# Kernel optimization log

Measured on AMD Instinct MI355X. Metric: run time of the kernel, lower is better.

The kernel has to match this reference:

```python
import jax, jax.numpy as jnp
import numpy as np

N_NODES = 50000
N_EDGES = 800000  # includes N_NODES self-loops so every node has in-degree >= 1
D_IN = 64
D_OUT = 64


def setup_inputs() -> dict:
    key = jax.random.key(0)
    k_feat, k_src, k_dst, k_wt, k_wp = jax.random.split(key, 5)
    feat = jax.random.normal(k_feat, (N_NODES, D_IN), dtype=jnp.float32)
    n_rand = N_EDGES - N_NODES
    loops = jnp.arange(N_NODES, dtype=jnp.int64)
    src = jnp.concatenate([loops, jax.random.randint(k_src, (n_rand,), 0, N_NODES, dtype=jnp.int64)])
    dst = jnp.concatenate([loops, jax.random.randint(k_dst, (n_rand,), 0, N_NODES, dtype=jnp.int64)])
    scale = 1.0 / np.sqrt(D_IN)
    W_theta = jax.random.normal(k_wt, (D_IN, D_OUT), dtype=jnp.float32) * scale
    b_theta = jnp.zeros((D_OUT,), dtype=jnp.float32)
    W_phi = jax.random.normal(k_wp, (D_IN, D_OUT), dtype=jnp.float32) * scale
    b_phi = jnp.zeros((D_OUT,), dtype=jnp.float32)
    return {"feat": feat, "src": src, "dst": dst,
            "W_theta": W_theta, "b_theta": b_theta,
            "W_phi": W_phi, "b_phi": b_phi}


def reference(feat, src, dst, W_theta, b_theta, W_phi, b_phi):
    # Per-edge message: theta(x_dst - x_src)  [fn.v_sub_u then Dense theta]
    diff = feat[dst] - feat[src]                       # [E, D_in]
    theta_e = diff @ W_theta + b_theta                 # [E, D_out]
    # Per-destination-node term: phi(x_dst)  [Dense phi]
    phi = feat @ W_phi + b_phi                         # [N, D_out]
    e = theta_e + phi[dst]                             # [E, D_out]  (fn.e_add_v)
    # Scatter-max aggregation by destination node (fn.max)
    out = jax.ops.segment_max(e, dst, num_segments=feat.shape[0])  # [N, D_out]
    return out
```

## Files before the change

### kernel.cpp

```cpp
#include <hip/hip_runtime.h>
#include <hip/hip_bf16.h>

#define N_NODES 50000
#define N_EDGES 800000
#define D 64
#define NB 391
#define BCAP 4096
#define CHUNK_E 2048
#define NSC 391
#define NSTRIP 3125
#define GEMM_BLKS 782

typedef __attribute__((ext_vector_type(8))) short short8v;
typedef __attribute__((ext_vector_type(4))) float float4v;

__device__ __forceinline__ float b2f(unsigned short h) {
    return __uint_as_float(((unsigned)h) << 16);
}
__device__ __forceinline__ unsigned short f2b(float f) {
    __hip_bfloat16 t = __float2bfloat16(f);
    return *reinterpret_cast<unsigned short*>(&t);
}
__device__ __forceinline__ short f2bs(float f) { return (short)f2b(f); }
__device__ __forceinline__ unsigned f2ord(float f) {
    unsigned u = __float_as_uint(f);
    return (u & 0x80000000u) ? ~u : (u | 0x80000000u);
}
__device__ __forceinline__ float ord2f(unsigned o) {
    return __uint_as_float((o & 0x80000000u) ? (o ^ 0x80000000u) : ~o);
}

__global__ __launch_bounds__(256)
void setup(const void* __restrict__ featv, const void* __restrict__ srcv,
           const void* __restrict__ Wtv, const void* __restrict__ btv,
           const void* __restrict__ Wpv, const void* __restrict__ bpv,
           unsigned* __restrict__ flags,
           unsigned short* __restrict__ WTfrag, unsigned short* __restrict__ WPfrag,
           float* __restrict__ bias_sum) {
    __shared__ unsigned sf[2];
    const int t = threadIdx.x;
    if (t < 64) {
        const unsigned short* p = (const unsigned short*)featv;
        float x = b2f(p[2 * t]);
        float a = fabsf(x);
        bool insane = !(a <= 64.f) || (x != 0.f && a < 9.3132e-10f);
        unsigned long long m = __ballot(insane);
        if (t == 0) sf[0] = (__popcll(m) >= 8) ? 1u : 0u;
    } else if (t < 128) {
        const int* s32 = (const int*)srcv;
        int v = s32[2 * (t - 64) + 1];
        unsigned long long m = __ballot(v == 0);
        if (t == 64) sf[1] = (__popcll(m) >= 32) ? 1u : 0u;
    }
    __syncthreads();
    const unsigned fp32mode = sf[0];
    if (t < 2) flags[t] = sf[t];
#pragma unroll
    for (int i = 0; i < 16; ++i) {
        int e = i * 256 + t;
        int k = e >> 6, n = e & 63;
        float vt, vp;
        if (fp32mode) {
            vt = ((const float*)Wtv)[e];
            vp = ((const float*)Wpv)[e];
        } else {
            vt = b2f(((const unsigned short*)Wtv)[e]);
            vp = b2f(((const unsigned short*)Wpv)[e]);
        }
        WTfrag[n * 64 + k] = f2b(vt);
        WPfrag[n * 64 + k] = f2b(vp);
    }
    if (t < 64) {
        if (fp32mode)
            bias_sum[t] = ((const float*)btv)[t] + ((const float*)bpv)[t];
        else
            bias_sum[t] = b2f(((const unsigned short*)btv)[t])
                        + b2f(((const unsigned short*)bpv)[t]);
    }
}

__global__ __launch_bounds__(256)
void gemm_scatter(const void* __restrict__ featv,
                  const unsigned short* __restrict__ WTfrag,
                  const unsigned short* __restrict__ WPfrag,
                  const float* __restrict__ bias_sum,
                  const void* __restrict__ srcv, const void* __restrict__ dstv,
                  const unsigned* __restrict__ flags,
                  unsigned* __restrict__ c_cur, unsigned* __restrict__ packed,
                  unsigned short* __restrict__ T16, void* __restrict__ outv) {
    const unsigned fp32mode = flags[0];
    if (blockIdx.x < GEMM_BLKS) {
        const int lane = threadIdx.x & 63;
        const int wid  = threadIdx.x >> 6;
        const int w = blockIdx.x * 4 + wid;
        if (w >= NSTRIP) return;
        const int m = lane & 15, q = lane >> 4;

        short8v A0, A1;
        if (fp32mode) {
            const float* fr = (const float*)featv + (w * 16 + m) * D + q * 8;
            float4 l0 = *(const float4*)(fr);
            float4 h0 = *(const float4*)(fr + 4);
            float4 l1 = *(const float4*)(fr + 32);
            float4 h1 = *(const float4*)(fr + 36);
            A0 = (short8v){f2bs(l0.x), f2bs(l0.y), f2bs(l0.z), f2bs(l0.w),
                           f2bs(h0.x), f2bs(h0.y), f2bs(h0.z), f2bs(h0.w)};
            A1 = (short8v){f2bs(l1.x), f2bs(l1.y), f2bs(l1.z), f2bs(l1.w),
                           f2bs(h1.x), f2bs(h1.y), f2bs(h1.z), f2bs(h1.w)};
        } else {
            const short* fr = (const short*)featv + (w * 16 + m) * D + q * 8;
            A0 = *(const short8v*)fr;
            A1 = *(const short8v*)(fr + 32);
        }

        const short8v* BT = (const short8v*)WTfrag;
        const short8v* BP = (const short8v*)WPfrag;
        float* Cf  = (float*)outv;
        unsigned short* Ch = (unsigned short*)outv;

#pragma unroll
        for (int c = 0; c < 4; ++c) {
            const int col = 16 * c + m;
            short8v Bt0 = BT[col * 8 + q];
            short8v Bt1 = BT[col * 8 + 4 + q];
            short8v Bp0 = BP[col * 8 + q];
            short8v Bp1 = BP[col * 8 + 4 + q];
            float bs = bias_sum[col];
            float4v accT = (float4v){0.f, 0.f, 0.f, 0.f};
            float4v accP = (float4v){bs, bs, bs, bs};
            accT = __builtin_amdgcn_mfma_f32_16x16x32_bf16(A0, Bt0, accT, 0, 0, 0);
            accT = __builtin_amdgcn_mfma_f32_16x16x32_bf16(A1, Bt1, accT, 0, 0, 0);
            accP = __builtin_amdgcn_mfma_f32_16x16x32_bf16(A0, Bp0, accP, 0, 0, 0);
            accP = __builtin_amdgcn_mfma_f32_16x16x32_bf16(A1, Bp1, accP, 0, 0, 0);
#pragma unroll
            for (int r = 0; r < 4; ++r) {
                const int row = w * 16 + q * 4 + r;
                T16[row * D + col] = f2b(accT[r]);
                if (fp32mode) Cf[row * D + col] = accT[r] + accP[r];
                else          Ch[row * D + col] = f2b(accT[r] + accP[r]);
            }
        }
    } else {
        __shared__ unsigned h[NB];
        const int t = threadIdx.x;
        for (int i = t; i < NB; i += 256) h[i] = 0;
        __syncthreads();
        const unsigned idx64 = flags[1];
        const int base = (blockIdx.x - GEMM_BLKS) * CHUNK_E;
        unsigned pk[CHUNK_E / 256];
#pragma unroll
        for (int j = 0; j < CHUNK_E / 256; ++j) {
            int e = base + j * 256 + t;
            unsigned p = 0xFFFFFFFFu;
            if (e < N_EDGES) {
                int s, d;
                if (idx64) {
                    s = (int)((const long long*)srcv)[e];
                    d = (int)((const long long*)dstv)[e];
                } else {
                    s = ((const int*)srcv)[e];
                    d = ((const int*)dstv)[e];
                }
                s = min(max(s, 0), N_NODES - 1);
                d = min(max(d, 0), N_NODES - 1);
                if (s != d) {
                    p = ((unsigned)d << 16) | (unsigned)s;
                    atomicAdd(&h[d >> 7], 1u);
                }
            }
            pk[j] = p;
        }
        __syncthreads();
        for (int i = t; i < NB; i += 256) h[i] = atomicAdd(&c_cur[i], h[i]);
        __syncthreads();
#pragma unroll
        for (int j = 0; j < CHUNK_E / 256; ++j) {
            unsigned p = pk[j];
            if (p != 0xFFFFFFFFu) {
                unsigned bkt = p >> 23;
                unsigned pos = atomicAdd(&h[bkt], 1u);
                if (pos < BCAP)
                    packed[bkt * BCAP + pos] = p;
            }
        }
    }
}

__global__ __launch_bounds__(512)
void bucket_min(const unsigned* __restrict__ c_cur, const unsigned* __restrict__ packed,
                const unsigned short* __restrict__ T16, const unsigned* __restrict__ flags,
                void* __restrict__ outv) {
    __shared__ unsigned mn[128 * 64];
    const unsigned fp32mode = flags[0];
    const int t = threadIdx.x;
    const int b = blockIdx.x;
    const int node0 = b << 7;
    for (int sl = t; sl < 128 * 16; sl += 512) {
        const int row = sl >> 4;
        const int f4 = (sl & 15) << 2;
        unsigned* mp = &mn[row * 64 + f4];
        if (node0 + row < N_NODES) {
            uint2 v = *(const uint2*)(T16 + (node0 + row) * D + f4);
            mp[0] = f2ord(b2f((unsigned short)v.x));
            mp[1] = f2ord(b2f((unsigned short)(v.x >> 16)));
            mp[2] = f2ord(b2f((unsigned short)v.y));
            mp[3] = f2ord(b2f((unsigned short)(v.y >> 16)));
        } else {
            mp[0] = mp[1] = mp[2] = mp[3] = 0xFFFFFFFFu;
        }
    }
    __syncthreads();
    const int cnt = min((int)c_cur[b], BCAP);
    const unsigned* pb = packed + b * BCAP;
    const int lane = t & 63, wv = t >> 6;
    const int g = lane >> 4, fb = (lane & 15) << 2;
    int i = wv * 4 + g;
    for (; i + 96 < cnt; i += 128) {
        unsigned p0 = pb[i],      p1 = pb[i + 32];
        unsigned p2 = pb[i + 64], p3 = pb[i + 96];
        uint2 v0 = *(const uint2*)(T16 + (int)(p0 & 0xFFFFu) * D + fb);
        uint2 v1 = *(const uint2*)(T16 + (int)(p1 & 0xFFFFu) * D + fb);
        uint2 v2 = *(const uint2*)(T16 + (int)(p2 & 0xFFFFu) * D + fb);
        uint2 v3 = *(const uint2*)(T16 + (int)(p3 & 0xFFFFu) * D + fb);
        unsigned* m0p = &mn[(int)((p0 >> 16) & 127u) * 64 + fb];
        unsigned* m1p = &mn[(int)((p1 >> 16) & 127u) * 64 + fb];
        unsigned* m2p = &mn[(int)((p2 >> 16) & 127u) * 64 + fb];
        unsigned* m3p = &mn[(int)((p3 >> 16) & 127u) * 64 + fb];
        atomicMin(m0p + 0, f2ord(b2f((unsigned short)v0.x)));
        atomicMin(m0p + 1, f2ord(b2f((unsigned short)(v0.x >> 16))));
        atomicMin(m0p + 2, f2ord(b2f((unsigned short)v0.y)));
        atomicMin(m0p + 3, f2ord(b2f((unsigned short)(v0.y >> 16))));
        atomicMin(m1p + 0, f2ord(b2f((unsigned short)v1.x)));
        atomicMin(m1p + 1, f2ord(b2f((unsigned short)(v1.x >> 16))));
        atomicMin(m1p + 2, f2ord(b2f((unsigned short)v1.y)));
        atomicMin(m1p + 3, f2ord(b2f((unsigned short)(v1.y >> 16))));
        atomicMin(m2p + 0, f2ord(b2f((unsigned short)v2.x)));
        atomicMin(m2p + 1, f2ord(b2f((unsigned short)(v2.x >> 16))));
        atomicMin(m2p + 2, f2ord(b2f((unsigned short)v2.y)));
        atomicMin(m2p + 3, f2ord(b2f((unsigned short)(v2.y >> 16))));
        atomicMin(m3p + 0, f2ord(b2f((unsigned short)v3.x)));
        atomicMin(m3p + 1, f2ord(b2f((unsigned short)(v3.x >> 16))));
        atomicMin(m3p + 2, f2ord(b2f((unsigned short)v3.y)));
        atomicMin(m3p + 3, f2ord(b2f((unsigned short)(v3.y >> 16))));
    }
    for (; i < cnt; i += 32) {
        unsigned p0 = pb[i];
        uint2 v0 = *(const uint2*)(T16 + (int)(p0 & 0xFFFFu) * D + fb);
        unsigned* m0p = &mn[(int)((p0 >> 16) & 127u) * 64 + fb];
        atomicMin(m0p + 0, f2ord(b2f((unsigned short)v0.x)));
        atomicMin(m0p + 1, f2ord(b2f((unsigned short)(v0.x >> 16))));
        atomicMin(m0p + 2, f2ord(b2f((unsigned short)v0.y)));
        atomicMin(m0p + 3, f2ord(b2f((unsigned short)(v0.y >> 16))));
    }
    __syncthreads();
    for (int sl = t; sl < 128 * 16; sl += 512) {
        const int row = sl >> 4;
        const int node = node0 + row;
        if (node >= N_NODES) break;
        const int f4 = (sl & 15) << 2;
        const unsigned* mp = &mn[row * 64 + f4];
        float m0 = ord2f(mp[0]), m1 = ord2f(mp[1]);
        float m2 = ord2f(mp[2]), m3 = ord2f(mp[3]);
        if (fp32mode) {
            float4* C = (float4*)((float*)outv + node * D + f4);
            float4 c = *C;
            *C = make_float4(c.x - m0, c.y - m1, c.z - m2, c.w - m3);
        } else {
            unsigned short* C = (unsigned short*)outv + node * D + f4;
            uint2 c = *(uint2*)C;
            unsigned lo = (unsigned)f2b(b2f((unsigned short)c.x) - m0)
                        | ((unsigned)f2b(b2f((unsigned short)(c.x >> 16)) - m1) << 16);
            unsigned hi = (unsigned)f2b(b2f((unsigned short)c.y) - m2)
                        | ((unsigned)f2b(b2f((unsigned short)(c.y >> 16)) - m3) << 16);
            *(uint2*)C = make_uint2(lo, hi);
        }
    }
}

extern "C" void kernel_launch(void* const* d_in, const int* in_sizes, int n_in,
                              void* d_out, int out_size, void* d_ws, size_t ws_size,
                              hipStream_t stream) {
    char* p = (char*)d_ws;
    unsigned*       flags    = (unsigned*)p;
    unsigned*       c_cur    = (unsigned*)(p + 256);
    unsigned*       packed   = (unsigned*)(p + 4352);
    unsigned short* T16      = (unsigned short*)(p + 4352 + 6406144);
    unsigned short* WTfrag   = (unsigned short*)(p + 4352 + 6406144 + 6400000);
    unsigned short* WPfrag   = (unsigned short*)(p + 4352 + 6406144 + 6400000 + 8192);
    float*          bias_sum = (float*)(p + 4352 + 6406144 + 6400000 + 16384);

    hipMemsetAsync(c_cur, 0, NB * sizeof(unsigned), stream);
    setup<<<1, 256, 0, stream>>>(d_in[0], d_in[1], d_in[3], d_in[4], d_in[5], d_in[6],
                                 flags, WTfrag, WPfrag, bias_sum);
    gemm_scatter<<<GEMM_BLKS + NSC, 256, 0, stream>>>(d_in[0], WTfrag, WPfrag, bias_sum,
                                                      d_in[1], d_in[2], flags,
                                                      c_cur, packed, T16, d_out);
    bucket_min<<<NB, 512, 0, stream>>>(c_cur, packed, T16, flags, d_out);
}
```

Before: 135.7 us.

## Make GEMM waves persistent over strips with prefetch; fold counter memset into setup

The GEMM part of the fused kernel now uses 196 blocks whose waves each loop over 4 strips. Weight fragments and bias are loaded once per wave and the next strip's features are prefetched during the current strip's work. The separate memset of the bucket counters is removed and the zeroing is done inside the setup kernel, which saves one launch. The bf16 path reloads the current A anyway, so that prefetch is partly redundant, and fewer GEMM blocks may reduce overlap with the scatter blocks.

```diff
diff --git a/kernel.cpp b/kernel.cpp
--- a/kernel.cpp
+++ b/kernel.cpp
@@ -9,7 +9,9 @@
 #define CHUNK_E 2048
 #define NSC 391
 #define NSTRIP 3125
-#define GEMM_BLKS 782
+#define GEMM_BLKS 196
+#define NWAVES 784
+#define SPW 4
 
 typedef __attribute__((ext_vector_type(8))) short short8v;
 typedef __attribute__((ext_vector_type(4))) float float4v;
@@ -34,7 +36,7 @@
 void setup(const void* __restrict__ featv, const void* __restrict__ srcv,
            const void* __restrict__ Wtv, const void* __restrict__ btv,
            const void* __restrict__ Wpv, const void* __restrict__ bpv,
-           unsigned* __restrict__ flags,
+           unsigned* __restrict__ flags, unsigned* __restrict__ c_cur,
            unsigned short* __restrict__ WTfrag, unsigned short* __restrict__ WPfrag,
            float* __restrict__ bias_sum) {
     __shared__ unsigned sf[2];
@@ -55,6 +57,7 @@
     __syncthreads();
     const unsigned fp32mode = sf[0];
     if (t < 2) flags[t] = sf[t];
+    for (int i = t; i < NB; i += 256) c_cur[i] = 0;
 #pragma unroll
     for (int i = 0; i < 16; ++i) {
         int e = i * 256 + t;
@@ -77,6 +80,25 @@
             bias_sum[t] = b2f(((const unsigned short*)btv)[t])
                         + b2f(((const unsigned short*)bpv)[t]);
     }
+}
+
+__device__ __forceinline__ void loadA_bf16(const short* F, int w, int m, int q,
+                                           short8v& A0, short8v& A1) {
+    const short* fr = F + (w * 16 + m) * D + q * 8;
+    A0 = *(const short8v*)fr;
+    A1 = *(const short8v*)(fr + 32);
+}
+__device__ __forceinline__ void loadA_raw(const float* F, int w, int m, int q,
+                                          float4 r[8]) {
+    const float* fr = F + (w * 16 + m) * D + q * 8;
+    r[0] = *(const float4*)(fr);      r[1] = *(const float4*)(fr + 4);
+    r[2] = *(const float4*)(fr + 32); r[3] = *(const float4*)(fr + 36);
+}
+__device__ __forceinline__ void cvtA(const float4 r[8], short8v& A0, short8v& A1) {
+    A0 = (short8v){f2bs(r[0].x), f2bs(r[0].y), f2bs(r[0].z), f2bs(r[0].w),
+                   f2bs(r[1].x), f2bs(r[1].y), f2bs(r[1].z), f2bs(r[1].w)};
+    A1 = (short8v){f2bs(r[2].x), f2bs(r[2].y), f2bs(r[2].z), f2bs(r[2].w),
+                   f2bs(r[3].x), f2bs(r[3].y), f2bs(r[3].z), f2bs(r[3].w)};
 }
 
 __global__ __launch_bounds__(256)
@@ -92,53 +114,70 @@
     if (blockIdx.x < GEMM_BLKS) {
         const int lane = threadIdx.x & 63;
         const int wid  = threadIdx.x >> 6;
-        const int w = blockIdx.x * 4 + wid;
-        if (w >= NSTRIP) return;
+        const int wave = blockIdx.x * 4 + wid;
         const int m = lane & 15, q = lane >> 4;
-
-        short8v A0, A1;
-        if (fp32mode) {
-            const float* fr = (const float*)featv + (w * 16 + m) * D + q * 8;
-            float4 l0 = *(const float4*)(fr);
-            float4 h0 = *(const float4*)(fr + 4);
-            float4 l1 = *(const float4*)(fr + 32);
-            float4 h1 = *(const float4*)(fr + 36);
-            A0 = (short8v){f2bs(l0.x), f2bs(l0.y), f2bs(l0.z), f2bs(l0.w),
-                           f2bs(h0.x), f2bs(h0.y), f2bs(h0.z), f2bs(h0.w)};
-            A1 = (short8v){f2bs(l1.x), f2bs(l1.y), f2bs(l1.z), f2bs(l1.w),
-                           f2bs(h1.x), f2bs(h1.y), f2bs(h1.z), f2bs(h1.w)};
-        } else {
-            const short* fr = (const short*)featv + (w * 16 + m) * D + q * 8;
-            A0 = *(const short8v*)fr;
-            A1 = *(const short8v*)(fr + 32);
-        }
 
         const short8v* BT = (const short8v*)WTfrag;
         const short8v* BP = (const short8v*)WPfrag;
+        short8v Bt0[4], Bt1[4], Bp0[4], Bp1[4];
+        float bsv[4];
+#pragma unroll
+        for (int c = 0; c < 4; ++c) {
+            const int col = 16 * c + m;
+            Bt0[c] = BT[col * 8 + q];
+            Bt1[c] = BT[col * 8 + 4 + q];
+            Bp0[c] = BP[col * 8 + q];
+            Bp1[c] = BP[col * 8 + 4 + q];
+            bsv[c] = bias_sum[col];
+        }
+
         float* Cf  = (float*)outv;
         unsigned short* Ch = (unsigned short*)outv;
-
-#pragma unroll
-        for (int c = 0; c < 4; ++c) {
-            const int col = 16 * c + m;
-            short8v Bt0 = BT[col * 8 + q];
-            short8v Bt1 = BT[col * 8 + 4 + q];
-            short8v Bp0 = BP[col * 8 + q];
-            short8v Bp1 = BP[col * 8 + 4 + q];
-            float bs = bias_sum[col];
-            float4v accT = (float4v){0.f, 0.f, 0.f, 0.f};
-            float4v accP = (float4v){bs, bs, bs, bs};
-            accT = __builtin_amdgcn_mfma_f32_16x16x32_bf16(A0, Bt0, accT, 0, 0, 0);
-            accT = __builtin_amdgcn_mfma_f32_16x16x32_bf16(A1, Bt1, accT, 0, 0, 0);
-            accP = __builtin_amdgcn_mfma_f32_16x16x32_bf16(A0, Bp0, accP, 0, 0, 0);
-            accP = __builtin_amdgcn_mfma_f32_16x16x32_bf16(A1, Bp1, accP, 0, 0, 0);
-#pragma unroll
-            for (int r = 0; r < 4; ++r) {
-                const int row = w * 16 + q * 4 + r;
-                T16[row * D + col] = f2b(accT[r]);
-                if (fp32mode) Cf[row * D + col] = accT[r] + accP[r];
-                else          Ch[row * D + col] = f2b(accT[r] + accP[r]);
+        const float* Ff = (const float*)featv;
+        const short* Fh = (const short*)featv;
+
+        short8v A0, A1;
+        float4 raw[8];
+        int w = wave;
+        if (fp32mode) { loadA_raw(Ff, min(w, NSTRIP - 1), m, q, raw); cvtA(raw, A0, A1); }
+        else          loadA_bf16(Fh, min(w, NSTRIP - 1), m, q, A0, A1);
+
+#pragma unroll
+        for (int s = 0; s < SPW; ++s) {
+            const int wn = wave + (s + 1) * NWAVES;
+            if (s + 1 < SPW) {
+                if (fp32mode) loadA_raw(Ff, min(wn, NSTRIP - 1), m, q, raw);
+                else          loadA_bf16(Fh, min(wn, NSTRIP - 1), m, q, A0, A1);
             }
+            if (w < NSTRIP) {
+                short8v Acur0, Acur1;
+                if (s + 1 < SPW && !fp32mode) {
+                    loadA_bf16(Fh, w, m, q, Acur0, Acur1);
+                } else if (!fp32mode) {
+                    Acur0 = A0; Acur1 = A1;
+                } else {
+                    Acur0 = A0; Acur1 = A1;
+                }
+#pragma unroll
+                for (int c = 0; c < 4; ++c) {
+                    float4v accT = (float4v){0.f, 0.f, 0.f, 0.f};
+                    float4v accP = (float4v){bsv[c], bsv[c], bsv[c], bsv[c]};
+                    accT = __builtin_amdgcn_mfma_f32_16x16x32_bf16(Acur0, Bt0[c], accT, 0, 0, 0);
+                    accT = __builtin_amdgcn_mfma_f32_16x16x32_bf16(Acur1, Bt1[c], accT, 0, 0, 0);
+                    accP = __builtin_amdgcn_mfma_f32_16x16x32_bf16(Acur0, Bp0[c], accP, 0, 0, 0);
+                    accP = __builtin_amdgcn_mfma_f32_16x16x32_bf16(Acur1, Bp1[c], accP, 0, 0, 0);
+                    const int col = 16 * c + m;
+#pragma unroll
+                    for (int r = 0; r < 4; ++r) {
+                        const int row = w * 16 + q * 4 + r;
+                        T16[row * D + col] = f2b(accT[r]);
+                        if (fp32mode) Cf[row * D + col] = accT[r] + accP[r];
+                        else          Ch[row * D + col] = f2b(accT[r] + accP[r]);
+                    }
+                }
+            }
+            w = wn;
+            if (fp32mode && s + 1 < SPW) cvtA(raw, A0, A1);
         }
     } else {
         __shared__ unsigned h[NB];
@@ -289,9 +328,8 @@
     unsigned short* WPfrag   = (unsigned short*)(p + 4352 + 6406144 + 6400000 + 8192);
     float*          bias_sum = (float*)(p + 4352 + 6406144 + 6400000 + 16384);
 
-    hipMemsetAsync(c_cur, 0, NB * sizeof(unsigned), stream);
     setup<<<1, 256, 0, stream>>>(d_in[0], d_in[1], d_in[3], d_in[4], d_in[5], d_in[6],
-                                 flags, WTfrag, WPfrag, bias_sum);
+                                 flags, c_cur, WTfrag, WPfrag, bias_sum);
     gemm_scatter<<<GEMM_BLKS + NSC, 256, 0, stream>>>(d_in[0], WTfrag, WPfrag, bias_sum,
                                                       d_in[1], d_in[2], flags,
                                                       c_cur, packed, T16, d_out);
```

Result: faster. 128.4 us (-5.4%).
